# Optimization experiments

Measured on AMD Instinct MI355X. Metric: run time of the kernel, lower is better.

Reference implementation:

```python
import jax, jax.numpy as jnp
import numpy as np

B, T, D_MODEL, H, DH = 4, 2048, 768, 12, 64


def _rope_tables(T, dh):
    # standard rotary frequencies, (T, dh//2)
    inv_freq = 1.0 / (10000.0 ** (np.arange(0, dh, 2, dtype=np.float32) / dh))
    t = np.arange(T, dtype=np.float32)
    ang = np.outer(t, inv_freq)  # (T, dh//2)
    return jnp.asarray(np.cos(ang)), jnp.asarray(np.sin(ang))


def setup_inputs() -> dict:
    key = jax.random.key(0)
    ks = jax.random.split(key, 5)
    scale = 1.0 / np.sqrt(D_MODEL)
    x = jax.random.normal(ks[0], (B, T, D_MODEL), dtype=jnp.float32)
    wq = jax.random.normal(ks[1], (D_MODEL, D_MODEL), dtype=jnp.float32) * scale
    wk = jax.random.normal(ks[2], (D_MODEL, D_MODEL), dtype=jnp.float32) * scale
    wv = jax.random.normal(ks[3], (D_MODEL, D_MODEL), dtype=jnp.float32) * scale
    wo = jax.random.normal(ks[4], (D_MODEL, D_MODEL), dtype=jnp.float32) * scale
    rope_cos, rope_sin = _rope_tables(T, DH)
    return {"x": x, "rope_cos": rope_cos, "rope_sin": rope_sin,
            "wq": wq, "wk": wk, "wv": wv, "wo": wo}


def _apply_rope(x, cos, sin):
    # x: (B, H, T, DH), cos/sin: (T, DH//2) -> interleaved rotation
    t = x.shape[2]
    c = cos[:t][None, None]  # (1,1,T,DH//2)
    s = sin[:t][None, None]
    x1 = x[..., ::2]
    x2 = x[..., 1::2]
    return jnp.stack([x1 * c - x2 * s, x1 * s + x2 * c], axis=-1).reshape(x.shape)


def reference(x, rope_cos, rope_sin, wq, wk, wv, wo):
    b, t, _ = x.shape
    # Linear (torch nn.Linear: y = x @ W.T), split heads -> (B,H,T,DH)
    q = (x @ wq.T).reshape(b, t, H, DH).transpose(0, 2, 1, 3)
    k = (x @ wk.T).reshape(b, t, H, DH).transpose(0, 2, 1, 3)
    v = (x @ wv.T).reshape(b, t, H, DH).transpose(0, 2, 1, 3)
    q = _apply_rope(q, rope_cos, rope_sin)
    k = _apply_rope(k, rope_cos, rope_sin)
    scores = jnp.einsum("bhqd,bhkd->bhqk", q, k) * (DH ** -0.5)
    causal = jnp.tril(jnp.ones((t, t), dtype=bool))  # (T,T)
    scores = jnp.where(causal[None, None], scores, -jnp.inf)
    attn = jax.nn.softmax(scores, axis=-1)
    out = jnp.einsum("bhqk,bhkd->bhqd", attn, v)
    out = out.transpose(0, 2, 1, 3).reshape(b, t, H * DH)
    return out @ wo.T
```

## Files before the change

### kernel.cpp

```cpp
#include <hip/hip_runtime.h>
#include <hip/hip_bf16.h>
#include <math.h>

#define B_ 4
#define T_ 2048
#define DM 768
#define H_ 12
#define DH 64

typedef __attribute__((ext_vector_type(4))) float f32x4;
typedef __attribute__((ext_vector_type(8))) short s16x8;

typedef const __attribute__((address_space(1))) void* gas1_t;
typedef __attribute__((address_space(3))) void* las3_t;

__device__ __forceinline__ ushort f2b(float f) {
  union { float f; unsigned u; } v; v.f = f;
  unsigned u = v.u;
  u += 0x7fffu + ((u >> 16) & 1u);
  return (ushort)(u >> 16);
}
__device__ __forceinline__ unsigned cvt_pk_bf16(float lo, float hi) {
  unsigned r;
  asm("v_cvt_pk_bf16_f32 %0, %1, %2" : "=v"(r) : "v"(lo), "v"(hi));
  return r;
}

__global__ void cvt_all(const float* __restrict__ x,
                        const float* __restrict__ wq, const float* __restrict__ wk,
                        const float* __restrict__ wv, const float* __restrict__ wo,
                        const float* __restrict__ rc, const float* __restrict__ rs,
                        ushort* __restrict__ xb, ushort* __restrict__ wqkv,
                        ushort* __restrict__ wob, float2* __restrict__ cs2) {
  const int bid = blockIdx.x, t = threadIdx.x;
  if (bid < 6144) {
    int i = bid * 256 + t;
    float4 v = ((const float4*)x)[i];
    ushort4 o;
    o.x = f2b(v.x); o.y = f2b(v.y); o.z = f2b(v.z); o.w = f2b(v.w);
    ((ushort4*)xb)[i] = o;
  } else if (bid < 8448) {
    int i = (bid - 6144) * 256 + t;
    int which = i / 147456, j = i - which * 147456;
    const float* src = which == 0 ? wq : which == 1 ? wk : which == 2 ? wv : wo;
    ushort* dst = which < 3 ? wqkv + (size_t)which * 589824 : wob;
    float4 v = ((const float4*)src)[j];
    ushort4 o;
    o.x = f2b(v.x); o.y = f2b(v.y); o.z = f2b(v.z); o.w = f2b(v.w);
    ((ushort4*)dst)[j] = o;
  } else {
    int i = (bid - 8448) * 256 + t;
    cs2[i] = make_float2(rc[i], rs[i]);
  }
}

__global__ __launch_bounds__(256, 3) void gemm_qkv(
    const ushort* __restrict__ A, const ushort* __restrict__ Bw,
    const float2* __restrict__ cs2,
    ushort* __restrict__ Qb, ushort* __restrict__ Kb, ushort* __restrict__ Vt) {
  const int K = 768;
  __shared__ ushort As[128 * 64];
  __shared__ ushort Bs[192 * 64];
  const int bid = blockIdx.x;
  const int xcd = bid & 7;
  const int jj = bid >> 3;
  const int mloc = jj / 12, nn0 = jj - mloc * 12;
  const int m0 = (xcd * 8 + mloc) * 128, n0 = nn0 * 192;
  const int tid = threadIdx.x;
  const int wave = tid >> 6, lane = tid & 63;
  const int wm = (wave >> 1) * 64, wn = (wave & 1) * 96;
  const int quad = lane >> 4, l16 = lane & 15;
  const int tr = tid >> 3;
  const int scb = (tid & 7) ^ (tr & 7);
  const int swz = l16 & 7;

  f32x4 acc[4][6] = {};

  const ushort* ga = A + (size_t)(m0 + tr) * K + scb * 8;
  const ushort* gb = Bw + (size_t)(n0 + tr) * K + scb * 8;

  for (int k0 = 0; k0 < K; k0 += 64) {
#pragma unroll
    for (int p = 0; p < 4; p++)
      __builtin_amdgcn_global_load_lds((gas1_t)(ga + (size_t)(p * 32) * K + k0),
                                       (las3_t)(As + p * 2048 + tid * 8), 16, 0, 0);
#pragma unroll
    for (int p = 0; p < 6; p++)
      __builtin_amdgcn_global_load_lds((gas1_t)(gb + (size_t)(p * 32) * K + k0),
                                       (las3_t)(Bs + p * 2048 + tid * 8), 16, 0, 0);
    __syncthreads();
#pragma unroll
    for (int kk = 0; kk < 2; kk++) {
      s16x8 af[4], bf[6];
#pragma unroll
      for (int i = 0; i < 4; i++) {
        const ushort* ar = As + (wm + i * 16 + l16) * 64;
        af[i] = *(const s16x8*)(ar + (((kk * 4 + quad) ^ swz) * 8));
      }
#pragma unroll
      for (int n = 0; n < 6; n++) {
        const ushort* br = Bs + (wn + n * 16 + l16) * 64;
        bf[n] = *(const s16x8*)(br + (((kk * 4 + quad) ^ swz) * 8));
      }
#pragma unroll
      for (int i = 0; i < 4; i++)
#pragma unroll
        for (int n = 0; n < 6; n++)
          acc[i][n] = __builtin_amdgcn_mfma_f32_16x16x32_bf16(af[i], bf[n], acc[i][n], 0, 0, 0);
    }
    __syncthreads();
  }

  const int sec = n0 / 768;
  if (sec < 2) {
    ushort* dst = sec == 0 ? Qb : Kb;
#pragma unroll
    for (int i = 0; i < 4; i++) {
      int row0 = m0 + wm + i * 16 + quad * 4;
#pragma unroll
      for (int nt = 0; nt < 6; nt++) {
        int col = n0 + wn + nt * 16 + l16;
        int nv = col - sec * 768;
        int h = nv >> 6, d = nv & 63;
        int ip = (d >> 1) & 31;
        float sgn = (d & 1) ? 1.f : -1.f;
#pragma unroll
        for (int r = 0; r < 4; r++) {
          int rrow = row0 + r;
          int t = rrow & (T_ - 1), bb = rrow >> 11;
          float v = acc[i][nt][r];
          float partner = __shfl_xor(v, 1);
          float2 cs = cs2[t * 32 + ip];
          float out = fmaf(v, cs.x, sgn * partner * cs.y);
          dst[((size_t)(bb * H_ + h) * T_ + t) * DH + d] = f2b(out);
        }
      }
    }
  } else {
#pragma unroll
    for (int i = 0; i < 4; i++) {
      int row0 = m0 + wm + i * 16 + quad * 4;
      int t0 = row0 & (T_ - 1), b = row0 >> 11;
#pragma unroll
      for (int nt = 0; nt < 6; nt++) {
        int col = n0 + wn + nt * 16 + l16;
        int nv = col - 1536;
        int h = nv >> 6, d = nv & 63;
        ushort4 pk;
        pk.x = f2b(acc[i][nt][0]); pk.y = f2b(acc[i][nt][1]);
        pk.z = f2b(acc[i][nt][2]); pk.w = f2b(acc[i][nt][3]);
        *(ushort4*)(Vt + ((size_t)(b * H_ + h) * DH + d) * T_ + t0) = pk;
      }
    }
  }
}

__global__ __launch_bounds__(256, 3) void gemm_out(
    const ushort* __restrict__ A, const ushort* __restrict__ Bw, float* __restrict__ C) {
  const int K = 768, N = 768;
  __shared__ ushort As[128 * 64];
  __shared__ ushort Bs[96 * 64];
  const int bid = blockIdx.x;
  const int xcd = bid & 7;
  const int jj = bid >> 3;
  const int mloc = jj >> 3, nn0 = jj & 7;
  const int m0 = (xcd * 8 + mloc) * 128, n0 = nn0 * 96;
  const int tid = threadIdx.x;
  const int wave = tid >> 6, lane = tid & 63;
  const int wm = (wave >> 1) * 64, wn = (wave & 1) * 48;
  const int quad = lane >> 4, l16 = lane & 15;
  const int tr = tid >> 3;
  const int scb = (tid & 7) ^ (tr & 7);
  const int swz = l16 & 7;

  f32x4 acc[4][3] = {};

  const ushort* ga = A + (size_t)(m0 + tr) * K + scb * 8;
  const ushort* gb = Bw + (size_t)(n0 + tr) * K + scb * 8;

  for (int k0 = 0; k0 < K; k0 += 64) {
#pragma unroll
    for (int p = 0; p < 4; p++)
      __builtin_amdgcn_global_load_lds((gas1_t)(ga + (size_t)(p * 32) * K + k0),
                                       (las3_t)(As + p * 2048 + tid * 8), 16, 0, 0);
#pragma unroll
    for (int p = 0; p < 3; p++)
      __builtin_amdgcn_global_load_lds((gas1_t)(gb + (size_t)(p * 32) * K + k0),
                                       (las3_t)(Bs + p * 2048 + tid * 8), 16, 0, 0);
    __syncthreads();
#pragma unroll
    for (int kk = 0; kk < 2; kk++) {
      s16x8 af[4], bf[3];
#pragma unroll
      for (int i = 0; i < 4; i++) {
        const ushort* ar = As + (wm + i * 16 + l16) * 64;
        af[i] = *(const s16x8*)(ar + (((kk * 4 + quad) ^ swz) * 8));
      }
#pragma unroll
      for (int n = 0; n < 3; n++) {
        const ushort* br = Bs + (wn + n * 16 + l16) * 64;
        bf[n] = *(const s16x8*)(br + (((kk * 4 + quad) ^ swz) * 8));
      }
#pragma unroll
      for (int i = 0; i < 4; i++)
#pragma unroll
        for (int n = 0; n < 3; n++)
          acc[i][n] = __builtin_amdgcn_mfma_f32_16x16x32_bf16(af[i], bf[n], acc[i][n], 0, 0, 0);
    }
    __syncthreads();
  }

#pragma unroll
  for (int i = 0; i < 4; i++) {
    int row = m0 + wm + i * 16 + quad * 4;
#pragma unroll
    for (int n = 0; n < 3; n++) {
      int col = n0 + wn + n * 16 + l16;
#pragma unroll
      for (int r = 0; r < 4; r++)
        C[(size_t)(row + r) * N + col] = acc[i][n][r];
    }
  }
}

#define EXP2SCALE 0.18033688f
#define EXP2OFF  17.312340f
__global__ __launch_bounds__(256, 3) void attn(const ushort* __restrict__ Qb, const ushort* __restrict__ Kb,
                                               const ushort* __restrict__ Vt, ushort* __restrict__ Ob) {
  const int bh = blockIdx.x;
  const int p = blockIdx.y;
  const int tid = threadIdx.x, wave = tid >> 6, lane = tid & 63;
  const int quad = lane >> 4, l16 = lane & 15;
  const int b = bh / H_, h = bh % H_;
  const ushort* Qp = Qb + (size_t)bh * T_ * DH;
  const ushort* Kp = Kb + (size_t)bh * T_ * DH;
  const ushort* Vp = Vt + (size_t)bh * DH * T_;

  __shared__ ushort Ks[2][64 * 64];
  __shared__ ushort Vs[2][64 * 64];
  __shared__ ushort P[4][16][64];

  const int myTile = (wave < 2) ? p : (63 - p);
  const int qb = myTile * 32 + (wave & 1) * 16;

  s16x8 aq[2];
  {
    const ushort* qp = Qp + (size_t)(qb + l16) * DH + quad * 8;
    aq[0] = *(const s16x8*)qp;
    aq[1] = *(const s16x8*)(qp + 32);
  }
  f32x4 o[4] = {};
  float rsum = 0.f;

  const int ntile = ((2047 - 32 * p) >> 6) + 1;
  const int srow = tid >> 3;
  const int scbK = (tid & 7) ^ (srow & 7);
  const int swz = (l16 & 7);
  const int psw = swz << 3;

  {
    const int kv0 = 0;
    __builtin_amdgcn_global_load_lds((gas1_t)(Kp + (size_t)(kv0 + srow) * DH + scbK * 8),
                                     (las3_t)(Ks[0] + tid * 8), 16, 0, 0);
    __builtin_amdgcn_global_load_lds((gas1_t)(Kp + (size_t)(kv0 + srow + 32) * DH + scbK * 8),
                                     (las3_t)(Ks[0] + 2048 + tid * 8), 16, 0, 0);
    __builtin_amdgcn_global_load_lds((gas1_t)(Vp + (size_t)srow * T_ + kv0 + scbK * 8),
                                     (las3_t)(Vs[0] + tid * 8), 16, 0, 0);
    __builtin_amdgcn_global_load_lds((gas1_t)(Vp + (size_t)(srow + 32) * T_ + kv0 + scbK * 8),
                                     (las3_t)(Vs[0] + 2048 + tid * 8), 16, 0, 0);
  }

  for (int c = 0; c < ntile; c++) {
    const int kv0 = c * 64;
    const int cur = c & 1;
    __syncthreads();
    if (c + 1 < ntile) {
      const int kv1 = kv0 + 64, nxt = cur ^ 1;
      __builtin_amdgcn_global_load_lds((gas1_t)(Kp + (size_t)(kv1 + srow) * DH + scbK * 8),
                                       (las3_t)(Ks[nxt] + tid * 8), 16, 0, 0);
      __builtin_amdgcn_global_load_lds((gas1_t)(Kp + (size_t)(kv1 + srow + 32) * DH + scbK * 8),
                                       (las3_t)(Ks[nxt] + 2048 + tid * 8), 16, 0, 0);
      __builtin_amdgcn_global_load_lds((gas1_t)(Vp + (size_t)srow * T_ + kv1 + scbK * 8),
                                       (las3_t)(Vs[nxt] + tid * 8), 16, 0, 0);
      __builtin_amdgcn_global_load_lds((gas1_t)(Vp + (size_t)(srow + 32) * T_ + kv1 + scbK * 8),
                                       (las3_t)(Vs[nxt] + 2048 + tid * 8), 16, 0, 0);
    }

    if (kv0 <= qb + 15) {
      s16x8 kf[4][2];
#pragma unroll
      for (int nt = 0; nt < 4; nt++) {
        const ushort* kr = Ks[cur] + (nt * 16 + l16) * 64;
        kf[nt][0] = *(const s16x8*)(kr + ((quad ^ swz) * 8));
        kf[nt][1] = *(const s16x8*)(kr + (((4 + quad) ^ swz) * 8));
      }
      s16x8 bv[4][2];
#pragma unroll
      for (int dt = 0; dt < 4; dt++) {
        const ushort* vr = Vs[cur] + (dt * 16 + l16) * 64;
        bv[dt][0] = *(const s16x8*)(vr + ((quad ^ swz) * 8));
        bv[dt][1] = *(const s16x8*)(vr + (((4 + quad) ^ swz) * 8));
      }

      f32x4 s[4] = {};
#pragma unroll
      for (int nt = 0; nt < 4; nt++) {
        s[nt] = __builtin_amdgcn_mfma_f32_16x16x32_bf16(kf[nt][0], aq[0], s[nt], 0, 0, 0);
        s[nt] = __builtin_amdgcn_mfma_f32_16x16x32_bf16(kf[nt][1], aq[1], s[nt], 0, 0, 0);
      }
      if (kv0 + 63 <= qb) {
#pragma unroll
        for (int nt = 0; nt < 4; nt++) {
          float p0 = __builtin_amdgcn_exp2f(fmaf(s[nt][0], EXP2SCALE, -EXP2OFF));
          float p1 = __builtin_amdgcn_exp2f(fmaf(s[nt][1], EXP2SCALE, -EXP2OFF));
          float p2 = __builtin_amdgcn_exp2f(fmaf(s[nt][2], EXP2SCALE, -EXP2OFF));
          float p3 = __builtin_amdgcn_exp2f(fmaf(s[nt][3], EXP2SCALE, -EXP2OFF));
          rsum += (p0 + p1) + (p2 + p3);
          int sc = (nt * 16 + quad * 4) ^ psw;
          uint2 pk;
          pk.x = cvt_pk_bf16(p0, p1);
          pk.y = cvt_pk_bf16(p2, p3);
          *(uint2*)&P[wave][l16][sc] = pk;
        }
      } else {
        int qi = qb + l16;
#pragma unroll
        for (int nt = 0; nt < 4; nt++) {
          int kvb = kv0 + nt * 16 + quad * 4;
          float pv[4];
#pragma unroll
          for (int r = 0; r < 4; r++)
            pv[r] = (kvb + r <= qi) ? __builtin_amdgcn_exp2f(fmaf(s[nt][r], EXP2SCALE, -EXP2OFF)) : 0.f;
          rsum += (pv[0] + pv[1]) + (pv[2] + pv[3]);
          int sc = (nt * 16 + quad * 4) ^ psw;
          uint2 pk;
          pk.x = cvt_pk_bf16(pv[0], pv[1]);
          pk.y = cvt_pk_bf16(pv[2], pv[3]);
          *(uint2*)&P[wave][l16][sc] = pk;
        }
      }
      s16x8 ap0 = *(const s16x8*)&P[wave][l16][(quad * 8) ^ psw];
      s16x8 ap1 = *(const s16x8*)&P[wave][l16][(32 + quad * 8) ^ psw];
#pragma unroll
      for (int dt = 0; dt < 4; dt++) {
        o[dt] = __builtin_amdgcn_mfma_f32_16x16x32_bf16(ap0, bv[dt][0], o[dt], 0, 0, 0);
        o[dt] = __builtin_amdgcn_mfma_f32_16x16x32_bf16(ap1, bv[dt][1], o[dt], 0, 0, 0);
      }
    }
  }
  rsum += __shfl_xor(rsum, 16);
  rsum += __shfl_xor(rsum, 32);
#pragma unroll
  for (int r = 0; r < 4; r++) {
    float inv = 1.0f / __shfl(rsum, quad * 4 + r);
    int q = qb + quad * 4 + r;
#pragma unroll
    for (int dt = 0; dt < 4; dt++)
      Ob[(size_t)(b * T_ + q) * DM + h * 64 + dt * 16 + l16] = f2b(o[dt][r] * inv);
  }
}

extern "C" void kernel_launch(void* const* d_in, const int* in_sizes, int n_in,
                              void* d_out, int out_size, void* d_ws, size_t ws_size,
                              hipStream_t stream) {
  const float* x = (const float*)d_in[0];
  const float* rc = (const float*)d_in[1];
  const float* rs = (const float*)d_in[2];
  const float* wq = (const float*)d_in[3];
  const float* wk = (const float*)d_in[4];
  const float* wv = (const float*)d_in[5];
  const float* wo = (const float*)d_in[6];

  char* ws = (char*)d_ws;
  ushort* xb   = (ushort*)(ws);
  ushort* wqkv = (ushort*)(ws + 12582912);
  ushort* wob  = (ushort*)(ws + 16121856);
  float2* cs2  = (float2*)(ws + 17301504);
  ushort* Qb   = (ushort*)(ws + 17825792);
  ushort* Kb   = (ushort*)(ws + 30408704);
  ushort* Vt   = (ushort*)(ws + 42991616);
  ushort* Ob   = (ushort*)(ws + 55574528);

  cvt_all<<<8704, 256, 0, stream>>>(x, wq, wk, wv, wo, rc, rs, xb, wqkv, wob, cs2);

  gemm_qkv<<<768, 256, 0, stream>>>(xb, wqkv, cs2, Qb, Kb, Vt);

  attn<<<dim3(48, 32), 256, 0, stream>>>(Qb, Kb, Vt, Ob);

  gemm_out<<<512, 256, 0, stream>>>(Ob, wob, (float*)d_out);
}
```

Before: 205.7 us.

## Run attention as two sequential 64-row query tiles per block with shared KV tiles

Each block previously held two 32-row query tiles (one from the front, one from the back) handled by different waves, so both streamed the full KV range and waves idled on masked tiles. Now all four waves work on the same 64-row query tile and the block processes tile p and then tile 31-p in sequence. This halves the grid, removes per-wave skipped iterations, and lets every loaded KV tile be used by all waves. The P scratch buffer also switches from an XOR swizzle to padding at 72 columns. The two phases run back to back, so the second phase pays its own pipeline prologue and there is less parallelism across the grid.

```diff
diff --git a/kernel.cpp b/kernel.cpp
--- a/kernel.cpp
+++ b/kernel.cpp
@@ -238,55 +238,56 @@
 
   __shared__ ushort Ks[2][64 * 64];
   __shared__ ushort Vs[2][64 * 64];
-  __shared__ ushort P[4][16][64];
-
-  const int myTile = (wave < 2) ? p : (63 - p);
-  const int qb = myTile * 32 + (wave & 1) * 16;
-
-  s16x8 aq[2];
-  {
-    const ushort* qp = Qp + (size_t)(qb + l16) * DH + quad * 8;
-    aq[0] = *(const s16x8*)qp;
-    aq[1] = *(const s16x8*)(qp + 32);
-  }
-  f32x4 o[4] = {};
-  float rsum = 0.f;
-
-  const int ntile = ((2047 - 32 * p) >> 6) + 1;
+  __shared__ ushort P[4][16][72];
+
   const int srow = tid >> 3;
   const int scbK = (tid & 7) ^ (srow & 7);
   const int swz = (l16 & 7);
-  const int psw = swz << 3;
-
-  {
-    const int kv0 = 0;
-    __builtin_amdgcn_global_load_lds((gas1_t)(Kp + (size_t)(kv0 + srow) * DH + scbK * 8),
-                                     (las3_t)(Ks[0] + tid * 8), 16, 0, 0);
-    __builtin_amdgcn_global_load_lds((gas1_t)(Kp + (size_t)(kv0 + srow + 32) * DH + scbK * 8),
-                                     (las3_t)(Ks[0] + 2048 + tid * 8), 16, 0, 0);
-    __builtin_amdgcn_global_load_lds((gas1_t)(Vp + (size_t)srow * T_ + kv0 + scbK * 8),
-                                     (las3_t)(Vs[0] + tid * 8), 16, 0, 0);
-    __builtin_amdgcn_global_load_lds((gas1_t)(Vp + (size_t)(srow + 32) * T_ + kv0 + scbK * 8),
-                                     (las3_t)(Vs[0] + 2048 + tid * 8), 16, 0, 0);
-  }
-
-  for (int c = 0; c < ntile; c++) {
-    const int kv0 = c * 64;
-    const int cur = c & 1;
-    __syncthreads();
-    if (c + 1 < ntile) {
-      const int kv1 = kv0 + 64, nxt = cur ^ 1;
-      __builtin_amdgcn_global_load_lds((gas1_t)(Kp + (size_t)(kv1 + srow) * DH + scbK * 8),
-                                       (las3_t)(Ks[nxt] + tid * 8), 16, 0, 0);
-      __builtin_amdgcn_global_load_lds((gas1_t)(Kp + (size_t)(kv1 + srow + 32) * DH + scbK * 8),
-                                       (las3_t)(Ks[nxt] + 2048 + tid * 8), 16, 0, 0);
-      __builtin_amdgcn_global_load_lds((gas1_t)(Vp + (size_t)srow * T_ + kv1 + scbK * 8),
-                                       (las3_t)(Vs[nxt] + tid * 8), 16, 0, 0);
-      __builtin_amdgcn_global_load_lds((gas1_t)(Vp + (size_t)(srow + 32) * T_ + kv1 + scbK * 8),
-                                       (las3_t)(Vs[nxt] + 2048 + tid * 8), 16, 0, 0);
-    }
-
-    if (kv0 <= qb + 15) {
+
+#pragma unroll
+  for (int phase = 0; phase < 2; phase++) {
+    const int tile = phase ? (31 - p) : p;
+    const int qb = tile * 64 + wave * 16;
+
+    s16x8 aq0, aq1;
+    {
+      const ushort* qp = Qp + (size_t)(qb + l16) * DH + quad * 8;
+      aq0 = *(const s16x8*)qp;
+      aq1 = *(const s16x8*)(qp + 32);
+    }
+    f32x4 o[4] = {};
+    float rsum = 0.f;
+    const int ntile = tile + 1;
+
+    __syncthreads();
+    {
+      const int kv0 = 0;
+      __builtin_amdgcn_global_load_lds((gas1_t)(Kp + (size_t)(kv0 + srow) * DH + scbK * 8),
+                                       (las3_t)(Ks[0] + tid * 8), 16, 0, 0);
+      __builtin_amdgcn_global_load_lds((gas1_t)(Kp + (size_t)(kv0 + srow + 32) * DH + scbK * 8),
+                                       (las3_t)(Ks[0] + 2048 + tid * 8), 16, 0, 0);
+      __builtin_amdgcn_global_load_lds((gas1_t)(Vp + (size_t)srow * T_ + kv0 + scbK * 8),
+                                       (las3_t)(Vs[0] + tid * 8), 16, 0, 0);
+      __builtin_amdgcn_global_load_lds((gas1_t)(Vp + (size_t)(srow + 32) * T_ + kv0 + scbK * 8),
+                                       (las3_t)(Vs[0] + 2048 + tid * 8), 16, 0, 0);
+    }
+
+    for (int c = 0; c < ntile; c++) {
+      const int kv0 = c * 64;
+      const int cur = c & 1;
+      __syncthreads();
+      if (c + 1 < ntile) {
+        const int kv1 = kv0 + 64, nxt = cur ^ 1;
+        __builtin_amdgcn_global_load_lds((gas1_t)(Kp + (size_t)(kv1 + srow) * DH + scbK * 8),
+                                         (las3_t)(Ks[nxt] + tid * 8), 16, 0, 0);
+        __builtin_amdgcn_global_load_lds((gas1_t)(Kp + (size_t)(kv1 + srow + 32) * DH + scbK * 8),
+                                         (las3_t)(Ks[nxt] + 2048 + tid * 8), 16, 0, 0);
+        __builtin_amdgcn_global_load_lds((gas1_t)(Vp + (size_t)srow * T_ + kv1 + scbK * 8),
+                                         (las3_t)(Vs[nxt] + tid * 8), 16, 0, 0);
+        __builtin_amdgcn_global_load_lds((gas1_t)(Vp + (size_t)(srow + 32) * T_ + kv1 + scbK * 8),
+                                         (las3_t)(Vs[nxt] + 2048 + tid * 8), 16, 0, 0);
+      }
+
       s16x8 kf[4][2];
 #pragma unroll
       for (int nt = 0; nt < 4; nt++) {
@@ -305,10 +306,10 @@
       f32x4 s[4] = {};
 #pragma unroll
       for (int nt = 0; nt < 4; nt++) {
-        s[nt] = __builtin_amdgcn_mfma_f32_16x16x32_bf16(kf[nt][0], aq[0], s[nt], 0, 0, 0);
-        s[nt] = __builtin_amdgcn_mfma_f32_16x16x32_bf16(kf[nt][1], aq[1], s[nt], 0, 0, 0);
-      }
-      if (kv0 + 63 <= qb) {
+        s[nt] = __builtin_amdgcn_mfma_f32_16x16x32_bf16(kf[nt][0], aq0, s[nt], 0, 0, 0);
+        s[nt] = __builtin_amdgcn_mfma_f32_16x16x32_bf16(kf[nt][1], aq1, s[nt], 0, 0, 0);
+      }
+      if (c < tile) {
 #pragma unroll
         for (int nt = 0; nt < 4; nt++) {
           float p0 = __builtin_amdgcn_exp2f(fmaf(s[nt][0], EXP2SCALE, -EXP2OFF));
@@ -316,11 +317,10 @@
           float p2 = __builtin_amdgcn_exp2f(fmaf(s[nt][2], EXP2SCALE, -EXP2OFF));
           float p3 = __builtin_amdgcn_exp2f(fmaf(s[nt][3], EXP2SCALE, -EXP2OFF));
           rsum += (p0 + p1) + (p2 + p3);
-          int sc = (nt * 16 + quad * 4) ^ psw;
           uint2 pk;
           pk.x = cvt_pk_bf16(p0, p1);
           pk.y = cvt_pk_bf16(p2, p3);
-          *(uint2*)&P[wave][l16][sc] = pk;
+          *(uint2*)&P[wave][l16][nt * 16 + quad * 4] = pk;
         }
       } else {
         int qi = qb + l16;
@@ -332,31 +332,31 @@
           for (int r = 0; r < 4; r++)
             pv[r] = (kvb + r <= qi) ? __builtin_amdgcn_exp2f(fmaf(s[nt][r], EXP2SCALE, -EXP2OFF)) : 0.f;
           rsum += (pv[0] + pv[1]) + (pv[2] + pv[3]);
-          int sc = (nt * 16 + quad * 4) ^ psw;
           uint2 pk;
           pk.x = cvt_pk_bf16(pv[0], pv[1]);
           pk.y = cvt_pk_bf16(pv[2], pv[3]);
-          *(uint2*)&P[wave][l16][sc] = pk;
+          *(uint2*)&P[wave][l16][nt * 16 + quad * 4] = pk;
         }
       }
-      s16x8 ap0 = *(const s16x8*)&P[wave][l16][(quad * 8) ^ psw];
-      s16x8 ap1 = *(const s16x8*)&P[wave][l16][(32 + quad * 8) ^ psw];
+      s16x8 ap0 = *(const s16x8*)&P[wave][l16][quad * 8];
+      s16x8 ap1 = *(const s16x8*)&P[wave][l16][32 + quad * 8];
 #pragma unroll
       for (int dt = 0; dt < 4; dt++) {
         o[dt] = __builtin_amdgcn_mfma_f32_16x16x32_bf16(ap0, bv[dt][0], o[dt], 0, 0, 0);
         o[dt] = __builtin_amdgcn_mfma_f32_16x16x32_bf16(ap1, bv[dt][1], o[dt], 0, 0, 0);
       }
     }
-  }
-  rsum += __shfl_xor(rsum, 16);
-  rsum += __shfl_xor(rsum, 32);
-#pragma unroll
-  for (int r = 0; r < 4; r++) {
-    float inv = 1.0f / __shfl(rsum, quad * 4 + r);
-    int q = qb + quad * 4 + r;
-#pragma unroll
-    for (int dt = 0; dt < 4; dt++)
-      Ob[(size_t)(b * T_ + q) * DM + h * 64 + dt * 16 + l16] = f2b(o[dt][r] * inv);
+
+    rsum += __shfl_xor(rsum, 16);
+    rsum += __shfl_xor(rsum, 32);
+#pragma unroll
+    for (int r = 0; r < 4; r++) {
+      float inv = 1.0f / __shfl(rsum, quad * 4 + r);
+      int q = qb + quad * 4 + r;
+#pragma unroll
+      for (int dt = 0; dt < 4; dt++)
+        Ob[(size_t)(b * T_ + q) * DM + h * 64 + dt * 16 + l16] = f2b(o[dt][r] * inv);
+    }
   }
 }
 
@@ -385,7 +385,7 @@
 
   gemm_qkv<<<768, 256, 0, stream>>>(xb, wqkv, cs2, Qb, Kb, Vt);
 
-  attn<<<dim3(48, 32), 256, 0, stream>>>(Qb, Kb, Vt, Ob);
+  attn<<<dim3(48, 16), 256, 0, stream>>>(Qb, Kb, Vt, Ob);
 
   gemm_out<<<512, 256, 0, stream>>>(Ob, wob, (float*)d_out);
 }
```

New measurement: 192.3 us. -6.5%, faster.
